# Kernel optimization log

Hardware: AMD Instinct MI355X
Metric: run time of the kernel (lower is better)

The kernel has to match this reference:

```python
import jax, jax.numpy as jnp
import numpy as np


def setup_inputs() -> dict:
    key = jax.random.key(0)
    ks = jax.random.split(key, 8)
    B, C, H, W = 4, 256, 64, 64
    Ci = C // 8  # inter_channels = 32
    x = jax.random.normal(ks[0], (B, C, H, W), dtype=jnp.float32)
    # 1x1 conv weights stored as [out, in] matrices (kernel size 1)
    sq = 1.0 / np.sqrt(C)
    Wq = jax.random.uniform(ks[1], (Ci, C), jnp.float32, -sq, sq)
    bq = jax.random.uniform(ks[2], (Ci,), jnp.float32, -sq, sq)
    Wk = jax.random.uniform(ks[3], (Ci, C), jnp.float32, -sq, sq)
    bk = jax.random.uniform(ks[4], (Ci,), jnp.float32, -sq, sq)
    Wv = jax.random.uniform(ks[5], (C, C), jnp.float32, -sq, sq)
    bv = jax.random.uniform(ks[6], (C,), jnp.float32, -sq, sq)
    # torch initializes gamma to zeros; use a nonzero value so output depends on attention path
    gamma = jnp.array([0.5], dtype=jnp.float32)
    return {"x": x, "Wq": Wq, "bq": bq, "Wk": Wk, "bk": bk, "Wv": Wv, "bv": bv, "gamma": gamma}


def reference(x, Wq, bq, Wk, bk, Wv, bv, gamma):
    B, C, H, W = x.shape
    N = H * W
    xf = x.reshape(B, C, N)                        # [B, C, N]
    # 1x1 convs == channel-mixing matmuls
    q = jnp.einsum('oc,bcn->bon', Wq, xf) + bq[None, :, None]   # [B, Ci, N]
    k = jnp.einsum('oc,bcn->bon', Wk, xf) + bk[None, :, None]   # [B, Ci, N]
    v = jnp.einsum('oc,bcn->bon', Wv, xf) + bv[None, :, None]   # [B, C,  N]
    # energy[b, n, m] = sum_c q[b, c, n] * k[b, c, m]  (no scaling, per DANet)
    energy = jnp.einsum('bcn,bcm->bnm', q, k)      # [B, N, N]
    attention = jax.nn.softmax(energy, axis=-1)    # softmax over keys m
    # out[b, c, n] = sum_m v[b, c, m] * attention[b, n, m]
    out = jnp.einsum('bcm,bnm->bcn', v, attention)
    out = out.reshape(B, C, H, W)
    return gamma[0] * out + x
```

## Files before the change

kernel.cpp:

```cpp
#include <hip/hip_runtime.h>
#include <hip/hip_bf16.h>
#include <math.h>

typedef __bf16 bf16x8 __attribute__((ext_vector_type(8)));
typedef float  floatx4 __attribute__((ext_vector_type(4)));
typedef float  floatx16 __attribute__((ext_vector_type(16)));
typedef unsigned u32x2 __attribute__((ext_vector_type(2)));

#define MFMA(a, b, c)   __builtin_amdgcn_mfma_f32_16x16x32_bf16((a), (b), (c), 0, 0, 0)
#define MFMA32(a, b, c) __builtin_amdgcn_mfma_f32_32x32x16_bf16((a), (b), (c), 0, 0, 0)

__device__ __forceinline__ unsigned short f2bf(float f) {
  union { float f; unsigned u; } v; v.f = f;
  unsigned r = v.u + 0x7FFFu + ((v.u >> 16) & 1u);
  return (unsigned short)(r >> 16);
}
__device__ __forceinline__ float bf2f(unsigned short u) {
  union { unsigned u; float f; } v; v.u = ((unsigned)u) << 16;
  return v.f;
}
__device__ __forceinline__ unsigned pack2(float a, float b) {
  __bf16 x = (__bf16)a, y = (__bf16)b;
  unsigned short ux = __builtin_bit_cast(unsigned short, x);
  unsigned short uy = __builtin_bit_cast(unsigned short, y);
  return (unsigned)ux | ((unsigned)uy << 16);
}
__device__ __forceinline__ float exp2_fast(float x) {
#if __has_builtin(__builtin_amdgcn_exp2f)
  return __builtin_amdgcn_exp2f(x);
#else
  return exp2f(x);
#endif
}

__global__ __launch_bounds__(256) void k_wconv(const float* __restrict__ Wq,
                                               const float* __restrict__ Wk,
                                               const float* __restrict__ Wv,
                                               unsigned short* __restrict__ Wall) {
  int i = blockIdx.x * 256 + threadIdx.x;
  int o = i >> 8, c = i & 255;
  float v = (o < 32) ? Wq[o * 256 + c]
          : (o < 64) ? Wk[(o - 32) * 256 + c]
                     : Wv[(o - 64) * 256 + c];
  Wall[i] = f2bf(v);
}

__global__ __launch_bounds__(256) void k_projx(const float* __restrict__ x,
                                               const unsigned short* __restrict__ Wall,
                                               const float* __restrict__ bq,
                                               const float* __restrict__ bk,
                                               const float* __restrict__ bv,
                                               unsigned short* __restrict__ qbf,
                                               unsigned short* __restrict__ kbf,
                                               unsigned short* __restrict__ vbf) {
  int b = blockIdx.x >> 7;
  int nb = blockIdx.x & 127;
  int n0 = nb * 32;
  int tid = threadIdx.x;
  int qr = tid >> 6;
  int lane = tid & 63;
  int l15 = lane & 15, quad = lane >> 4;

  __shared__ alignas(16) unsigned short xs[32][264];
  __shared__ alignas(16) unsigned short Os[4][64][24];

  {
    int g = tid & 7;
    int r0 = tid >> 3;
    const float* xcol = x + (size_t)b * 256 * 4096 + n0 + g * 4;
#pragma unroll
    for (int pass = 0; pass < 8; ++pass) {
      int r = pass * 32 + r0;
      float4 d = *(const float4*)(xcol + (size_t)r * 4096);
      xs[g * 4 + 0][r] = f2bf(d.x);
      xs[g * 4 + 1][r] = f2bf(d.y);
      xs[g * 4 + 2][r] = f2bf(d.z);
      xs[g * 4 + 3][r] = f2bf(d.w);
    }
  }
  __syncthreads();

#pragma unroll
  for (int ms = 0; ms < 2; ++ms) {
    int m0 = n0 + ms * 16;

    floatx4 acc[5];
#pragma unroll
    for (int tt = 0; tt < 5; ++tt) acc[tt] = floatx4{0.f, 0.f, 0.f, 0.f};

#pragma unroll
    for (int ks = 0; ks < 8; ++ks) {
      bf16x8 a = *(const bf16x8*)&xs[ms * 16 + l15][ks * 32 + quad * 8];
      {
        bf16x8 w = *(const bf16x8*)(Wall + (size_t)(qr * 16 + l15) * 256 + ks * 32 + quad * 8);
        acc[0] = MFMA(a, w, acc[0]);
      }
#pragma unroll
      for (int t = 0; t < 4; ++t) {
        int gt = 4 + qr * 4 + t;
        bf16x8 w = *(const bf16x8*)(Wall + (size_t)(gt * 16 + l15) * 256 + ks * 32 + quad * 8);
        acc[1 + t] = MFMA(a, w, acc[1 + t]);
      }
    }
    {
      int o = qr * 16 + l15;
      float bias = (o < 32) ? bq[o] : bk[o - 32];
      float scale = (o < 32) ? 1.44269504088896340736f : 1.0f;
      unsigned short* dst = (o < 32) ? qbf : kbf;
      int oc = o & 31;
      int kh = oc >> 4, h2 = (oc >> 3) & 1, c8 = oc & 7;
#pragma unroll
      for (int r = 0; r < 4; ++r) {
        int m = m0 + quad * 4 + r;
        dst[(size_t)b * 131072 + (size_t)(m >> 5) * 1024 + kh * 512 + h2 * 256 +
            (m & 31) * 8 + c8] = f2bf((acc[0][r] + bias) * scale);
      }
    }
#pragma unroll
    for (int t = 0; t < 4; ++t) {
      int lr = t * 16 + l15;
      int c = qr * 64 + lr;
      float bias = bv[c];
#pragma unroll
      for (int r = 0; r < 4; ++r)
        Os[qr][lr][quad * 4 + r] = f2bf(acc[1 + t][r] + bias);
    }
    {
      int kb = nb, kk = ms;
#pragma unroll
      for (int i = 0; i < 2; ++i) {
        int idx = lane + 64 * i;
        int r = idx >> 1, g = idx & 1;
        int c = qr * 64 + r;
        int cb = c >> 5, ch = c & 31;
        *(uint4*)(vbf + (size_t)b * 1048576 + (size_t)kb * 8192 +
                  (size_t)cb * 1024 + kk * 512 + g * 256 + ch * 8) =
            *(const uint4*)&Os[qr][r][g * 8];
      }
    }
  }
}

__device__ __forceinline__ void softmax_pack(floatx16 st, float& lp, bf16x8 (&pa)[2], int hi) {
  float p[16];
#pragma unroll
  for (int r = 0; r < 16; ++r) p[r] = exp2_fast(st[r]);
  lp += (((p[0] + p[1]) + (p[2] + p[3])) + ((p[4] + p[5]) + (p[6] + p[7]))) +
        (((p[8] + p[9]) + (p[10] + p[11])) + ((p[12] + p[13]) + (p[14] + p[15])));
  unsigned d0[4], d1[4];
#pragma unroll
  for (int t = 0; t < 4; ++t) {
    d0[t] = pack2(p[4 * t + 0], p[4 * t + 1]);
    d1[t] = pack2(p[4 * t + 2], p[4 * t + 3]);
  }
#pragma unroll
  for (int ks = 0; ks < 2; ++ks) {
#if __has_builtin(__builtin_amdgcn_permlane32_swap)
    (void)hi;
    u32x2 r0 = __builtin_amdgcn_permlane32_swap(d0[2 * ks], d0[2 * ks + 1], false, false);
    u32x2 r1 = __builtin_amdgcn_permlane32_swap(d1[2 * ks], d1[2 * ks + 1], false, false);
    union { unsigned u[4]; bf16x8 v; } u;
    u.u[0] = r0[0]; u.u[1] = r1[0]; u.u[2] = r0[1]; u.u[3] = r1[1];
    pa[ks] = u.v;
#else
    unsigned s0 = hi ? d0[2 * ks] : d0[2 * ks + 1];
    unsigned s1 = hi ? d1[2 * ks] : d1[2 * ks + 1];
    unsigned o0 = (unsigned)__shfl_xor((int)s0, 32);
    unsigned o1 = (unsigned)__shfl_xor((int)s1, 32);
    union { unsigned u[4]; bf16x8 v; } u;
    u.u[0] = hi ? o0 : d0[2 * ks];
    u.u[1] = hi ? o1 : d1[2 * ks];
    u.u[2] = hi ? d0[2 * ks + 1] : o0;
    u.u[3] = hi ? d1[2 * ks + 1] : o1;
    pa[ks] = u.v;
#endif
  }
}

__global__ __launch_bounds__(256, 2) void k_attn(const unsigned short* __restrict__ qbf,
                                                 const unsigned short* __restrict__ kbf,
                                                 const unsigned short* __restrict__ vbf,
                                                 const float* __restrict__ x,
                                                 const float* __restrict__ gma,
                                                 float* __restrict__ out) {
  int wg = (blockIdx.x & 7) * 64 + (blockIdx.x >> 3);
  const int qb = wg & 63;
  const int g  = wg >> 6;
  const int cw = g & 1;
  const int b  = g >> 1;
  const int s  = threadIdx.x >> 6;
  const int lane = threadIdx.x & 63;
  const int l31 = lane & 31;
  const int hi  = lane >> 5;
  const int q0  = qb * 64;

  __shared__ float lpL[4][64];
  __shared__ float ltot[64];
  __shared__ alignas(16) unsigned short Ol[4][128][40];

  const floatx16 z16 = {0.f, 0.f, 0.f, 0.f, 0.f, 0.f, 0.f, 0.f,
                        0.f, 0.f, 0.f, 0.f, 0.f, 0.f, 0.f, 0.f};

  bf16x8 qf[2][2];
  {
    const unsigned short* qbase =
        qbf + (size_t)b * 131072 + (size_t)(qb * 2) * 1024 + hi * 256 + l31 * 8;
#pragma unroll
    for (int qs2 = 0; qs2 < 2; ++qs2)
#pragma unroll
      for (int kh = 0; kh < 2; ++kh)
        qf[qs2][kh] = *(const bf16x8*)(qbase + qs2 * 1024 + kh * 512);
  }

  floatx16 acc[2][4];
#pragma unroll
  for (int i = 0; i < 2; ++i)
#pragma unroll
    for (int j = 0; j < 4; ++j) acc[i][j] = z16;

  float lp0 = 0.f, lp1 = 0.f;

  const unsigned short* krow =
      kbf + (size_t)b * 131072 + (size_t)(s * 32) * 1024 + hi * 256 + l31 * 8;
  const unsigned short* vrow =
      vbf + (size_t)b * 1048576 + (size_t)(s * 32) * 8192 + (size_t)(cw * 4) * 1024 +
      hi * 256 + l31 * 8;

  bf16x8 kf0 = *(const bf16x8*)krow;
  bf16x8 kf1 = *(const bf16x8*)(krow + 512);
  floatx16 st0 = MFMA32(kf0, qf[0][0], z16);
  st0 = MFMA32(kf1, qf[0][1], st0);
  floatx16 st1 = MFMA32(kf0, qf[1][0], z16);
  st1 = MFMA32(kf1, qf[1][1], st1);
  kf0 = *(const bf16x8*)(krow + 1024);
  kf1 = *(const bf16x8*)(krow + 1024 + 512);

  for (int it = 0; it < 32; ++it) {
    bf16x8 vb[4][2];
    const unsigned short* vit = vrow + (size_t)it * 8192;
#pragma unroll
    for (int ct = 0; ct < 4; ++ct) {
      vb[ct][0] = *(const bf16x8*)(vit + ct * 1024);
      vb[ct][1] = *(const bf16x8*)(vit + ct * 1024 + 512);
    }

    bf16x8 pa[2][2];
    softmax_pack(st0, lp0, pa[0], hi);
    softmax_pack(st1, lp1, pa[1], hi);

    st0 = MFMA32(kf0, qf[0][0], z16);
    st0 = MFMA32(kf1, qf[0][1], st0);
    st1 = MFMA32(kf0, qf[1][0], z16);
    st1 = MFMA32(kf1, qf[1][1], st1);

    const unsigned short* kn = krow + (size_t)((it + 2) & 31) * 1024;
    kf0 = *(const bf16x8*)kn;
    kf1 = *(const bf16x8*)(kn + 512);

    __builtin_amdgcn_s_setprio(1);
#pragma unroll
    for (int ct = 0; ct < 4; ++ct) {
      acc[0][ct] = MFMA32(pa[0][0], vb[ct][0], acc[0][ct]);
      acc[1][ct] = MFMA32(pa[1][0], vb[ct][0], acc[1][ct]);
      acc[0][ct] = MFMA32(pa[0][1], vb[ct][1], acc[0][ct]);
      acc[1][ct] = MFMA32(pa[1][1], vb[ct][1], acc[1][ct]);
    }
    __builtin_amdgcn_s_setprio(0);
  }

  lp0 += __shfl_xor(lp0, 32);
  lp1 += __shfl_xor(lp1, 32);
  lpL[s][hi * 32 + l31] = hi ? lp1 : lp0;
  __syncthreads();
  if (threadIdx.x < 64) {
    int q = threadIdx.x;
    ltot[q] = (lpL[0][q] + lpL[1][q]) + (lpL[2][q] + lpL[3][q]);
  }
  const float gv = gma[0];

#pragma unroll
  for (int qs2 = 0; qs2 < 2; ++qs2) {
#pragma unroll
    for (int ct = 0; ct < 4; ++ct) {
#pragma unroll
      for (int gi = 0; gi < 4; ++gi) {
        unsigned w0 = pack2(acc[qs2][ct][4 * gi + 0], acc[qs2][ct][4 * gi + 1]);
        unsigned w1 = pack2(acc[qs2][ct][4 * gi + 2], acc[qs2][ct][4 * gi + 3]);
        unsigned long long w = (unsigned long long)w0 | ((unsigned long long)w1 << 32);
        *(unsigned long long*)&Ol[s][ct * 32 + l31][8 * gi + 4 * hi] = w;
      }
    }
    __syncthreads();
    {
      int ch = threadIdx.x >> 1;
      int qh = threadIdx.x & 1;
      int qoff = qs2 * 32 + qh * 16;
      float o[16];
#pragma unroll
      for (int j = 0; j < 16; ++j) o[j] = 0.f;
#pragma unroll
      for (int sp = 0; sp < 4; ++sp) {
        const uint4* p = (const uint4*)&Ol[sp][ch][qh * 16];
        uint4 a0 = p[0], a1 = p[1];
        unsigned uu[8] = {a0.x, a0.y, a0.z, a0.w, a1.x, a1.y, a1.z, a1.w};
#pragma unroll
        for (int jj = 0; jj < 8; ++jj) {
          o[2 * jj + 0] += bf2f((unsigned short)(uu[jj] & 0xffffu));
          o[2 * jj + 1] += bf2f((unsigned short)(uu[jj] >> 16));
        }
      }
      size_t rowa = ((size_t)b * 256 + cw * 128 + ch) * 4096 + q0 + qoff;
      const float* xrow = x + rowa;
      float* orow = out + rowa;
#pragma unroll
      for (int j4 = 0; j4 < 4; ++j4) {
        float4 xv = *(const float4*)(xrow + j4 * 4);
        float4 r;
        r.x = xv.x + gv * o[j4 * 4 + 0] / ltot[qoff + j4 * 4 + 0];
        r.y = xv.y + gv * o[j4 * 4 + 1] / ltot[qoff + j4 * 4 + 1];
        r.z = xv.z + gv * o[j4 * 4 + 2] / ltot[qoff + j4 * 4 + 2];
        r.w = xv.w + gv * o[j4 * 4 + 3] / ltot[qoff + j4 * 4 + 3];
        *(float4*)(orow + j4 * 4) = r;
      }
    }
    __syncthreads();
  }
}

extern "C" void kernel_launch(void* const* d_in, const int* in_sizes, int n_in,
                              void* d_out, int out_size, void* d_ws, size_t ws_size,
                              hipStream_t stream) {
  const float* x   = (const float*)d_in[0];
  const float* Wq  = (const float*)d_in[1];
  const float* bq  = (const float*)d_in[2];
  const float* Wk  = (const float*)d_in[3];
  const float* bk  = (const float*)d_in[4];
  const float* Wv  = (const float*)d_in[5];
  const float* bv  = (const float*)d_in[6];
  const float* gma = (const float*)d_in[7];
  float* out = (float*)d_out;

  unsigned short* qbf  = (unsigned short*)d_ws;
  unsigned short* kbf  = qbf + (size_t)4 * 131072;
  unsigned short* vbf  = kbf + (size_t)4 * 131072;
  unsigned short* Wall = vbf + (size_t)4 * 1048576;

  k_wconv<<<320, 256, 0, stream>>>(Wq, Wk, Wv, Wall);
  k_projx<<<512, 256, 0, stream>>>(x, Wall, bq, bk, bv, qbf, kbf, vbf);
  k_attn<<<512, 256, 0, stream>>>(qbf, kbf, vbf, x, gma, out);
}
```

Measured before the change: 155.8 us.

## Retile attention: 128 queries by 64 channels per block, Q staged in LDS

Changes the per-block tile from 64 queries by 128 channels to 128 queries by 64 channels, so each block covers 32 query blocks times 4 channel quarters. Q fragments now live in shared memory and are reloaded every iteration, and scores are computed in the same iteration as the PV MFMAs. This drops the software pipelining of QK^T one step ahead. The intent is to halve V loads per query and increase the QK work relative to V traffic, at the cost of recomputing the scores four times across channel quarters instead of twice, and of losing the score prefetch overlap.

Result: slower. 181.4 us (+16.4%).

```diff
diff --git a/kernel.cpp b/kernel.cpp
--- a/kernel.cpp
+++ b/kernel.cpp
@@ -184,146 +184,140 @@
                                                  const float* __restrict__ gma,
                                                  float* __restrict__ out) {
   int wg = (blockIdx.x & 7) * 64 + (blockIdx.x >> 3);
-  const int qb = wg & 63;
-  const int g  = wg >> 6;
-  const int cw = g & 1;
-  const int b  = g >> 1;
-  const int s  = threadIdx.x >> 6;
-  const int lane = threadIdx.x & 63;
+  const int qb = wg & 31;
+  const int g  = wg >> 5;
+  const int cz = g & 3;
+  const int b  = g >> 2;
+  const int tid = threadIdx.x;
+  const int s  = tid >> 6;
+  const int lane = tid & 63;
   const int l31 = lane & 31;
   const int hi  = lane >> 5;
-  const int q0  = qb * 64;
-
-  __shared__ float lpL[4][64];
-  __shared__ float ltot[64];
-  __shared__ alignas(16) unsigned short Ol[4][128][40];
+  const int q0  = qb * 128;
+
+  __shared__ alignas(16) unsigned short SH[4 * 64 * 136];
+  __shared__ float lpL[4][128];
+  __shared__ float ltot[128];
 
   const floatx16 z16 = {0.f, 0.f, 0.f, 0.f, 0.f, 0.f, 0.f, 0.f,
                         0.f, 0.f, 0.f, 0.f, 0.f, 0.f, 0.f, 0.f};
 
-  bf16x8 qf[2][2];
   {
-    const unsigned short* qbase =
-        qbf + (size_t)b * 131072 + (size_t)(qb * 2) * 1024 + hi * 256 + l31 * 8;
-#pragma unroll
-    for (int qs2 = 0; qs2 < 2; ++qs2)
-#pragma unroll
-      for (int kh = 0; kh < 2; ++kh)
-        qf[qs2][kh] = *(const bf16x8*)(qbase + qs2 * 1024 + kh * 512);
-  }
-
-  floatx16 acc[2][4];
-#pragma unroll
-  for (int i = 0; i < 2; ++i)
-#pragma unroll
-    for (int j = 0; j < 4; ++j) acc[i][j] = z16;
-
-  float lp0 = 0.f, lp1 = 0.f;
+    const unsigned short* qsrc = qbf + (size_t)b * 131072 + (size_t)(qb * 4) * 1024;
+    *(uint4*)&SH[tid * 16 + 0] = *(const uint4*)(qsrc + tid * 16 + 0);
+    *(uint4*)&SH[tid * 16 + 8] = *(const uint4*)(qsrc + tid * 16 + 8);
+  }
+  __syncthreads();
+
+  floatx16 acc[4][2];
+#pragma unroll
+  for (int i = 0; i < 4; ++i)
+#pragma unroll
+    for (int j = 0; j < 2; ++j) acc[i][j] = z16;
+
+  float lpq[4] = {0.f, 0.f, 0.f, 0.f};
 
   const unsigned short* krow =
       kbf + (size_t)b * 131072 + (size_t)(s * 32) * 1024 + hi * 256 + l31 * 8;
   const unsigned short* vrow =
-      vbf + (size_t)b * 1048576 + (size_t)(s * 32) * 8192 + (size_t)(cw * 4) * 1024 +
+      vbf + (size_t)b * 1048576 + (size_t)(s * 32) * 8192 + (size_t)(cz * 2) * 1024 +
       hi * 256 + l31 * 8;
 
   bf16x8 kf0 = *(const bf16x8*)krow;
   bf16x8 kf1 = *(const bf16x8*)(krow + 512);
-  floatx16 st0 = MFMA32(kf0, qf[0][0], z16);
-  st0 = MFMA32(kf1, qf[0][1], st0);
-  floatx16 st1 = MFMA32(kf0, qf[1][0], z16);
-  st1 = MFMA32(kf1, qf[1][1], st1);
-  kf0 = *(const bf16x8*)(krow + 1024);
-  kf1 = *(const bf16x8*)(krow + 1024 + 512);
+  const int qoffL = hi * 256 + l31 * 8;
 
   for (int it = 0; it < 32; ++it) {
-    bf16x8 vb[4][2];
+    bf16x8 vb[2][2];
     const unsigned short* vit = vrow + (size_t)it * 8192;
 #pragma unroll
-    for (int ct = 0; ct < 4; ++ct) {
+    for (int ct = 0; ct < 2; ++ct) {
       vb[ct][0] = *(const bf16x8*)(vit + ct * 1024);
       vb[ct][1] = *(const bf16x8*)(vit + ct * 1024 + 512);
     }
 
-    bf16x8 pa[2][2];
-    softmax_pack(st0, lp0, pa[0], hi);
-    softmax_pack(st1, lp1, pa[1], hi);
-
-    st0 = MFMA32(kf0, qf[0][0], z16);
-    st0 = MFMA32(kf1, qf[0][1], st0);
-    st1 = MFMA32(kf0, qf[1][0], z16);
-    st1 = MFMA32(kf1, qf[1][1], st1);
-
-    const unsigned short* kn = krow + (size_t)((it + 2) & 31) * 1024;
+    bf16x8 pa[4][2];
+#pragma unroll
+    for (int qs = 0; qs < 4; ++qs) {
+      bf16x8 q0f = *(const bf16x8*)&SH[qs * 1024 + qoffL];
+      bf16x8 q1f = *(const bf16x8*)&SH[qs * 1024 + 512 + qoffL];
+      floatx16 st = MFMA32(kf0, q0f, z16);
+      st = MFMA32(kf1, q1f, st);
+      softmax_pack(st, lpq[qs], pa[qs], hi);
+    }
+
+    const unsigned short* kn = krow + (size_t)((it + 1) & 31) * 1024;
     kf0 = *(const bf16x8*)kn;
     kf1 = *(const bf16x8*)(kn + 512);
 
     __builtin_amdgcn_s_setprio(1);
 #pragma unroll
-    for (int ct = 0; ct < 4; ++ct) {
-      acc[0][ct] = MFMA32(pa[0][0], vb[ct][0], acc[0][ct]);
-      acc[1][ct] = MFMA32(pa[1][0], vb[ct][0], acc[1][ct]);
-      acc[0][ct] = MFMA32(pa[0][1], vb[ct][1], acc[0][ct]);
-      acc[1][ct] = MFMA32(pa[1][1], vb[ct][1], acc[1][ct]);
-    }
+    for (int qs = 0; qs < 4; ++qs)
+#pragma unroll
+      for (int ct = 0; ct < 2; ++ct) {
+        acc[qs][ct] = MFMA32(pa[qs][0], vb[ct][0], acc[qs][ct]);
+        acc[qs][ct] = MFMA32(pa[qs][1], vb[ct][1], acc[qs][ct]);
+      }
     __builtin_amdgcn_s_setprio(0);
   }
 
-  lp0 += __shfl_xor(lp0, 32);
-  lp1 += __shfl_xor(lp1, 32);
-  lpL[s][hi * 32 + l31] = hi ? lp1 : lp0;
+#pragma unroll
+  for (int qs = 0; qs < 4; ++qs) {
+    lpq[qs] += __shfl_xor(lpq[qs], 32);
+    if (hi == 0) lpL[s][qs * 32 + l31] = lpq[qs];
+  }
   __syncthreads();
-  if (threadIdx.x < 64) {
-    int q = threadIdx.x;
-    ltot[q] = (lpL[0][q] + lpL[1][q]) + (lpL[2][q] + lpL[3][q]);
-  }
-  const float gv = gma[0];
-
-#pragma unroll
-  for (int qs2 = 0; qs2 < 2; ++qs2) {
-#pragma unroll
-    for (int ct = 0; ct < 4; ++ct) {
+
+#pragma unroll
+  for (int qs = 0; qs < 4; ++qs)
+#pragma unroll
+    for (int ct = 0; ct < 2; ++ct)
 #pragma unroll
       for (int gi = 0; gi < 4; ++gi) {
-        unsigned w0 = pack2(acc[qs2][ct][4 * gi + 0], acc[qs2][ct][4 * gi + 1]);
-        unsigned w1 = pack2(acc[qs2][ct][4 * gi + 2], acc[qs2][ct][4 * gi + 3]);
+        unsigned w0 = pack2(acc[qs][ct][4 * gi + 0], acc[qs][ct][4 * gi + 1]);
+        unsigned w1 = pack2(acc[qs][ct][4 * gi + 2], acc[qs][ct][4 * gi + 3]);
         unsigned long long w = (unsigned long long)w0 | ((unsigned long long)w1 << 32);
-        *(unsigned long long*)&Ol[s][ct * 32 + l31][8 * gi + 4 * hi] = w;
-      }
-    }
-    __syncthreads();
-    {
-      int ch = threadIdx.x >> 1;
-      int qh = threadIdx.x & 1;
-      int qoff = qs2 * 32 + qh * 16;
-      float o[16];
-#pragma unroll
-      for (int j = 0; j < 16; ++j) o[j] = 0.f;
-#pragma unroll
-      for (int sp = 0; sp < 4; ++sp) {
-        const uint4* p = (const uint4*)&Ol[sp][ch][qh * 16];
-        uint4 a0 = p[0], a1 = p[1];
-        unsigned uu[8] = {a0.x, a0.y, a0.z, a0.w, a1.x, a1.y, a1.z, a1.w};
-#pragma unroll
-        for (int jj = 0; jj < 8; ++jj) {
-          o[2 * jj + 0] += bf2f((unsigned short)(uu[jj] & 0xffffu));
-          o[2 * jj + 1] += bf2f((unsigned short)(uu[jj] >> 16));
+        *(unsigned long long*)&SH[((size_t)(s * 64) + ct * 32 + l31) * 136 +
+                                  qs * 32 + 8 * gi + 4 * hi] = w;
+      }
+  if (tid < 128)
+    ltot[tid] = (lpL[0][tid] + lpL[1][tid]) + (lpL[2][tid] + lpL[3][tid]);
+  __syncthreads();
+
+  {
+    const float gv = gma[0];
+    int ch = tid >> 2;
+    int qg = tid & 3;
+    float o[32];
+#pragma unroll
+    for (int j = 0; j < 32; ++j) o[j] = 0.f;
+#pragma unroll
+    for (int sp = 0; sp < 4; ++sp) {
+      const unsigned short* prow = &SH[((size_t)(sp * 64) + ch) * 136 + qg * 32];
+#pragma unroll
+      for (int u = 0; u < 4; ++u) {
+        uint4 a = *(const uint4*)(prow + u * 8);
+        unsigned uu[4] = {a.x, a.y, a.z, a.w};
+#pragma unroll
+        for (int jj = 0; jj < 4; ++jj) {
+          o[u * 8 + 2 * jj + 0] += bf2f((unsigned short)(uu[jj] & 0xffffu));
+          o[u * 8 + 2 * jj + 1] += bf2f((unsigned short)(uu[jj] >> 16));
         }
       }
-      size_t rowa = ((size_t)b * 256 + cw * 128 + ch) * 4096 + q0 + qoff;
-      const float* xrow = x + rowa;
-      float* orow = out + rowa;
-#pragma unroll
-      for (int j4 = 0; j4 < 4; ++j4) {
-        float4 xv = *(const float4*)(xrow + j4 * 4);
-        float4 r;
-        r.x = xv.x + gv * o[j4 * 4 + 0] / ltot[qoff + j4 * 4 + 0];
-        r.y = xv.y + gv * o[j4 * 4 + 1] / ltot[qoff + j4 * 4 + 1];
-        r.z = xv.z + gv * o[j4 * 4 + 2] / ltot[qoff + j4 * 4 + 2];
-        r.w = xv.w + gv * o[j4 * 4 + 3] / ltot[qoff + j4 * 4 + 3];
-        *(float4*)(orow + j4 * 4) = r;
-      }
-    }
-    __syncthreads();
+    }
+    size_t rowa = ((size_t)b * 256 + cz * 64 + ch) * 4096 + q0 + qg * 32;
+    const float* xrow = x + rowa;
+    float* orow = out + rowa;
+#pragma unroll
+    for (int j4 = 0; j4 < 8; ++j4) {
+      float4 xv = *(const float4*)(xrow + j4 * 4);
+      float4 r;
+      r.x = xv.x + gv * o[j4 * 4 + 0] / ltot[qg * 32 + j4 * 4 + 0];
+      r.y = xv.y + gv * o[j4 * 4 + 1] / ltot[qg * 32 + j4 * 4 + 1];
+      r.z = xv.z + gv * o[j4 * 4 + 2] / ltot[qg * 32 + j4 * 4 + 2];
+      r.w = xv.w + gv * o[j4 * 4 + 3] / ltot[qg * 32 + j4 * 4 + 3];
+      *(float4*)(orow + j4 * 4) = r;
+    }
   }
 }
 
```
